# Performance work log

Measured on AMD Instinct MI355X. Metric: run time of the kernel, lower is better.

Reference implementation:

```python
import jax, jax.numpy as jnp
import numpy as np

B, R, H, W = 128, 8, 256, 256


def _conv(x, w, b):
    # x: [1, C_in, h, w], w: [C_out, C_in, 3, 3]; stride 2, pad 1, then bias + ReLU
    y = jax.lax.conv_general_dilated(
        x, w, window_strides=(2, 2), padding=((1, 1), (1, 1)),
        dimension_numbers=('NCHW', 'OIHW', 'NCHW'))
    return jax.nn.relu(y + b[None, :, None, None])


def _single(x, w1, b1, w2, b2, w3, b3, fw, fb):
    # x: [3, H, W]; one sample through its region's CNN expert
    h = x[None]                      # [1,3,H,W]
    h = _conv(h, w1, b1)             # [1,32,H/2,W/2]
    h = _conv(h, w2, b2)             # [1,64,H/4,W/4]
    h = _conv(h, w3, b3)             # [1,128,H/8,W/8]
    feat = h.mean(axis=(2, 3))[0]    # [128] global average pool
    return fw @ feat + fb            # [num_classes]


def setup_inputs() -> dict:
    key = jax.random.key(0)
    ks = jax.random.split(key, 10)
    s = 0.05
    return {
        'image': jax.random.normal(ks[0], (B, 3, H, W), jnp.float32),
        'region': jax.random.randint(ks[1], (B,), 0, R, jnp.int64),
        'w1': jax.random.normal(ks[2], (R, 32, 3, 3, 3), jnp.float32) * s,
        'b1': jax.random.normal(ks[3], (R, 32), jnp.float32) * s,
        'w2': jax.random.normal(ks[4], (R, 64, 32, 3, 3), jnp.float32) * s,
        'b2': jax.random.normal(ks[5], (R, 64), jnp.float32) * s,
        'w3': jax.random.normal(ks[6], (R, 128, 64, 3, 3), jnp.float32) * s,
        'b3': jax.random.normal(ks[7], (R, 128), jnp.float32) * s,
        'fw': jax.random.normal(ks[8], (R, 2, 128), jnp.float32) * s,
        'fb': jax.random.normal(ks[9], (R, 2), jnp.float32) * s,
    }


def reference(image, region, w1, b1, w2, b2, w3, b3, fw, fb):
    # MoE-style dispatch: gather each sample's region weights, vmap per-sample expert.
    r = region.astype(jnp.int32)
    pw = [jnp.take(p, r, axis=0) for p in (w1, b1, w2, b2, w3, b3, fw, fb)]
    out = jax.vmap(_single)(image, *pw)  # [B, num_classes]
    return out
```

## Files before the change

### kernel.cpp

```cpp
#include <hip/hip_runtime.h>
#include <cstdint>


typedef __attribute__((ext_vector_type(8))) short short8;
typedef __attribute__((ext_vector_type(4))) float floatx4;
typedef __attribute__((ext_vector_type(4))) unsigned short ushort4v;
typedef __attribute__((ext_vector_type(4))) float float4v;

__device__ inline unsigned short f2bf(float f) {
  union { float f; unsigned u; } x;
  x.f = f;
  unsigned u = x.u;
  u += 0x7FFFu + ((u >> 16) & 1u);
  return (unsigned short)(u >> 16);
}

__device__ inline void g2l16(const unsigned short* g, unsigned short* l) {
  __builtin_amdgcn_global_load_lds(
      (const __attribute__((address_space(1))) unsigned int*)g,
      (__attribute__((address_space(3))) unsigned int*)(unsigned int)(uintptr_t)l,
      16, 0, 0);
}

__global__ __launch_bounds__(256) void setup_k(
    const int* __restrict__ rp, int* __restrict__ rout, float* __restrict__ feat,
    const float* __restrict__ w1, unsigned short* __restrict__ w1p,
    const float* __restrict__ w2, unsigned short* __restrict__ w2p,
    const float* __restrict__ w3, unsigned short* __restrict__ w3p,
    unsigned short* __restrict__ h2p, int nhalo) {
  const int tid = threadIdx.x;
  if (blockIdx.x == 0) {
    __shared__ int is64;
    if (tid == 0) {
      int odd_or = 0;
      for (int i = 0; i < 64; ++i) odd_or |= rp[2 * i + 1];
      is64 = (odd_or == 0) ? 1 : 0;
    }
    __syncthreads();
    if (tid < 128) {
      int r = is64 ? rp[2 * tid] : rp[tid];
      rout[tid] = r & 7;
      float* fr = feat + tid * 128;
      for (int j = 0; j < 128; ++j) fr[j] = 0.f;
    }
    return;
  }
  int t = (blockIdx.x - 1) * 256 + tid;
  if (t < 16384) {
    int j = t & 7, lane = (t >> 3) & 63, mt = (t >> 9) & 1, kg = (t >> 10) & 1,
        r = t >> 11;
    int oc = mt * 16 + (lane & 15);
    int q = (lane >> 4) & 3;
    int row = kg * 2 + (q >> 1);
    int idx = (q & 1) * 8 + j;
    int kx = idx >> 2, c = idx & 3;
    float val = 0.f;
    if (row < 3 && kx < 3 && c < 3)
      val = w1[((r * 32 + oc) * 3 + c) * 9 + row * 3 + kx];
    w1p[t] = f2bf(val);
  } else if (t < 163840) {
    int t2 = t - 16384;
    int j = t2 & 7, lane = (t2 >> 3) & 63;
    int u = t2 >> 9;
    int mt = u & 3; u >>= 2;
    int tap = u % 9;
    int r = u / 9;
    int oc = mt * 16 + (lane & 15);
    int ic = ((lane >> 4) & 3) * 8 + j;
    w2p[t2] = f2bf(w2[((r * 64 + oc) * 32 + ic) * 9 + tap]);
  } else if (t < 753664) {
    int t3 = t - 163840;
    int j = t3 & 7, lane = (t3 >> 3) & 63;
    int u = t3 >> 9;
    int mt = u & 7; u >>= 3;
    int s = u & 1; u >>= 1;
    int tap = u % 9;
    int r = u / 9;
    int oc = mt * 16 + (lane & 15);
    int ic = s * 32 + ((lane >> 4) & 3) * 8 + j;
    w3p[t3] = f2bf(w3[((r * 128 + oc) * 64 + ic) * 9 + tap]);
  } else {
    int th = t - 753664;
    if (th < nhalo) {
      int s = th / 260, i = th - s * 260;
      int y, x;
      if (i < 66) { y = 0; x = i; }
      else if (i < 132) { y = 65; x = i - 66; }
      else {
        int ii = i - 132;
        y = 1 + (ii >> 1);
        x = (ii & 1) ? 65 : 0;
      }
      short8 z = {0, 0, 0, 0, 0, 0, 0, 0};
      *(short8*)(h2p + ((size_t)s * 66 * 66 + y * 66 + x) * 8) = z;
    }
  }
}

__global__ __launch_bounds__(256, 3) void conv12_k(
    const float* __restrict__ img, const unsigned short* __restrict__ w1p,
    const float* __restrict__ b1, const unsigned short* __restrict__ w2p,
    const float* __restrict__ b2, const int* __restrict__ rgn,
    unsigned short* __restrict__ outp, int b0) {
  __shared__ unsigned short imgT[11 * 168 * 4];
  __shared__ unsigned short h1T[9 * 4 * 66 * 8];
  __shared__ float sB1[32];
  __shared__ float sB2[64];
  const int tid = threadIdx.x;
  const int xh = blockIdx.x;
  const int oy0 = blockIdx.y * 4;
  const int bl = blockIdx.z;
  const int r = __builtin_amdgcn_readfirstlane(rgn[b0 + bl]);
  if (tid < 32) sB1[tid] = b1[r * 32 + tid];
  if (tid >= 64 && tid < 128) sB2[tid - 64] = b2[r * 64 + (tid - 64)];
  const float* ib = img + (size_t)(b0 + bl) * 3 * 65536;
  const int padx = xh ? 65 : 0;
  const bool skiptop = (oy0 == 0);
  const int rb = xh * 128 - 4;

  const int n = tid & 15, q = (tid >> 4) & 3, wv = tid >> 6;
  const int lane = tid & 63;
  const short8* wpb1 = (const short8*)w1p + (size_t)r * 256 + lane;
  short8 afr1[2][2];
#pragma unroll
  for (int kg = 0; kg < 2; ++kg)
#pragma unroll
    for (int m = 0; m < 2; ++m) afr1[kg][m] = wpb1[(kg * 2 + m) * 64];

  auto STAGE = [&](int t0, int nrows) {
    const int nch = nrows * 41;
    for (int seg = 0; seg < nch; seg += 256) {
      int c = seg + tid;
      if (c < nch) {
        int i = c / 41, cq = c - i * 41;
        int rv = 4 * oy0 - 3 + t0 + i;
        int cb = rb + 4 * cq;
        unsigned short* dp = &imgT[((size_t)i * 168 + (4 * cq - 1)) * 4];
        if (rv >= 0 && cq > 0 && cb >= 0 && cb + 3 <= 255) {
          const float* p = ib + (size_t)rv * 256 + cb;
          float4v a = *(const float4v*)p;
          float4v bb = *(const float4v*)(p + 65536);
          float4v cc = *(const float4v*)(p + 131072);
#pragma unroll
          for (int e = 0; e < 4; ++e) {
            ushort4v v = {f2bf(a[e]), f2bf(bb[e]), f2bf(cc[e]), 0};
            *(ushort4v*)(dp + e * 4) = v;
          }
        } else {
          for (int e = (cq == 0 ? 1 : 0); e < 4; ++e) {
            int cc2 = cb + e;
            ushort4v v = {0, 0, 0, 0};
            if (rv >= 0 && cc2 >= 0 && cc2 <= 255) {
              const float* p = ib + (size_t)rv * 256 + cc2;
              v.x = f2bf(p[0]);
              v.y = f2bf(p[65536]);
              v.z = f2bf(p[131072]);
            }
            *(ushort4v*)(dp + e * 4) = v;
          }
        }
      }
    }
  };

  auto CONV1ROW = [&](int hy, int phaseB) {
    floatx4 a1[5][2];
#pragma unroll
    for (int nt = 0; nt < 5; ++nt)
#pragma unroll
      for (int m = 0; m < 2; ++m) a1[nt][m] = (floatx4){0.f, 0.f, 0.f, 0.f};
#pragma unroll
    for (int kg = 0; kg < 2; ++kg) {
      int row = kg * 2 + (q >> 1);
      int rowc = (row < 3) ? row : 0;
      int tr = 2 * hy + rowc;
      int slot = phaseB ? (tr >= 11 ? tr - 11 : tr) : tr;
#pragma unroll
      for (int nt = 0; nt < 5; ++nt) {
        int lx = nt * 16 + n;
        short8 bfr = *(const short8*)&imgT[((size_t)slot * 168 + 2 * lx) * 4 +
                                           (q & 1) * 8];
#pragma unroll
        for (int m = 0; m < 2; ++m)
          a1[nt][m] = __builtin_amdgcn_mfma_f32_16x16x32_bf16(
              afr1[kg][m], bfr, a1[nt][m], 0, 0, 0);
      }
    }
#pragma unroll
    for (int nt = 0; nt < 5; ++nt) {
      int lx = nt * 16 + n;
      bool ok = (lx <= 65) && (lx != padx) && !(skiptop && hy == 0);
      if (ok) {
#pragma unroll
        for (int m = 0; m < 2; ++m) {
          ushort4v st;
#pragma unroll
          for (int rr = 0; rr < 4; ++rr) {
            float v = a1[nt][m][rr] + sB1[m * 16 + q * 4 + rr];
            st[rr] = f2bf(v > 0.f ? v : 0.f);
          }
          int cg = m * 2 + (q >> 1);
          *(ushort4v*)&h1T[(((size_t)hy * 4 + cg) * 66 + lx) * 8 +
                           (q & 1) * 4] = st;
        }
      }
    }
  };

  STAGE(0, 11);
  {
    short8 z8 = {0, 0, 0, 0, 0, 0, 0, 0};
    if (tid < 36) {
      int hy = tid / 4, cg = tid % 4;
      *(short8*)&h1T[(((size_t)hy * 4 + cg) * 66 + padx) * 8] = z8;
    }
    if (skiptop) {
      for (int c = tid; c < 264; c += 256) {
        int cg = c / 66, x = c - cg * 66;
        *(short8*)&h1T[(((size_t)0 * 4 + cg) * 66 + x) * 8] = z8;
      }
    }
  }
  __syncthreads();

  for (int hy = wv; hy <= 4; hy += 4) CONV1ROW(hy, 0);
  __syncthreads();

  STAGE(11, 8);
  __syncthreads();

  CONV1ROW(5 + wv, 1);
  __syncthreads();

  const short8* wpb2 = (const short8*)w2p + (size_t)r * 9 * 4 * 64 + lane;
  floatx4 a2[2][4];
#pragma unroll
  for (int nt = 0; nt < 2; ++nt)
#pragma unroll
    for (int m = 0; m < 4; ++m) a2[nt][m] = (floatx4){0.f, 0.f, 0.f, 0.f};
#pragma unroll
  for (int tap = 0; tap < 9; ++tap) {
    const int ky = tap / 3, kx = tap % 3;
    short8 af[4];
#pragma unroll
    for (int m = 0; m < 4; ++m) af[m] = wpb2[(tap * 4 + m) * 64];
    short8 bf[2];
#pragma unroll
    for (int nt = 0; nt < 2; ++nt) {
      int ox = nt * 16 + n;
      bf[nt] = *(const short8*)&h1T[((((2 * wv + ky) << 2) + q) * 66 +
                                    (2 * ox + kx)) * 8];
    }
#pragma unroll
    for (int m = 0; m < 4; ++m)
#pragma unroll
      for (int nt = 0; nt < 2; ++nt)
        a2[nt][m] = __builtin_amdgcn_mfma_f32_16x16x32_bf16(af[m], bf[nt],
                                                            a2[nt][m], 0, 0, 0);
  }
  unsigned short* ob = outp + (size_t)bl * 8 * 66 * 66 * 8;
  const int oy = oy0 + wv;
#pragma unroll
  for (int nt = 0; nt < 2; ++nt) {
    int ox = xh * 32 + nt * 16 + n;
#pragma unroll
    for (int m = 0; m < 4; ++m) {
      ushort4v st;
#pragma unroll
      for (int rr = 0; rr < 4; ++rr) {
        float v = a2[nt][m][rr] + sB2[m * 16 + q * 4 + rr];
        st[rr] = f2bf(v > 0.f ? v : 0.f);
      }
      int cg = m * 2 + (q >> 1);
      *(ushort4v*)&ob[(((size_t)cg * 66 + oy + 1) * 66 + ox + 1) * 8 +
                      (q & 1) * 4] = st;
    }
  }
}

__global__ __launch_bounds__(256, 2) void conv3f_k(
    const unsigned short* __restrict__ in, const unsigned short* __restrict__ wp,
    const float* __restrict__ bias, const int* __restrict__ rgn,
    float* __restrict__ feat, int b0) {
  __shared__ unsigned short tile[9 * 8 * 66 * 8];
  __shared__ float sBias[128];
  __shared__ float sGap[4 * 128];
  const int tid = threadIdx.x;
  const int bl = blockIdx.y;
  const int b = b0 + bl;
  const int r = __builtin_amdgcn_readfirstlane(rgn[b]);
  if (tid < 128) sBias[tid] = bias[r * 128 + tid];
  const int oy0 = blockIdx.x * 4;
  const unsigned short* gbase = in + (size_t)bl * 8 * 66 * 66 * 8;
  const int lane = tid & 63, wv = tid >> 6;
  const int n = lane & 15, q = (lane >> 4) & 3;

  for (int seg = 0; seg < 4752; seg += 256) {
    int c = seg + tid;
    if (c < 4752) {
      int iy = c / 528;
      int rem = c - iy * 528;
      int c8 = rem / 66;
      int x = rem - c8 * 66;
      const unsigned short* gp =
          gbase + (((size_t)c8 * 66 + 2 * oy0 + iy) * 66 + x) * 8;
      g2l16(gp, tile + (size_t)(seg + wv * 64) * 8);
    }
  }
  __syncthreads();

  const short8* wpb = (const short8*)wp + (size_t)r * 9 * 2 * 8 * 64 + lane;
  floatx4 acc[2][8];
#pragma unroll
  for (int nt = 0; nt < 2; ++nt)
#pragma unroll
    for (int m = 0; m < 8; ++m) acc[nt][m] = (floatx4){0.f, 0.f, 0.f, 0.f};

#pragma unroll
  for (int s = 0; s < 2; ++s)
#pragma unroll
    for (int tap = 0; tap < 9; ++tap) {
      const int ky = tap / 3, kx = tap % 3;
      short8 afr[8];
#pragma unroll
      for (int m = 0; m < 8; ++m) afr[m] = wpb[((tap * 2 + s) * 8 + m) * 64];
      short8 bfr[2];
#pragma unroll
      for (int nt = 0; nt < 2; ++nt) {
        int ox = nt * 16 + n;
        bfr[nt] = *(const short8*)&tile[((((2 * wv + ky) * 8) + s * 4 + q) * 66 +
                                        (2 * ox + kx)) * 8];
      }
#pragma unroll
      for (int m = 0; m < 8; ++m)
#pragma unroll
        for (int nt = 0; nt < 2; ++nt)
          acc[nt][m] = __builtin_amdgcn_mfma_f32_16x16x32_bf16(afr[m], bfr[nt],
                                                               acc[nt][m], 0, 0, 0);
    }

#pragma unroll
  for (int m = 0; m < 8; ++m)
#pragma unroll
    for (int rr = 0; rr < 4; ++rr) {
      float bv = sBias[m * 16 + q * 4 + rr];
      float vs = 0.f;
#pragma unroll
      for (int nt = 0; nt < 2; ++nt) {
        float v = acc[nt][m][rr] + bv;
        vs += (v > 0.f ? v : 0.f);
      }
      vs += __shfl_xor(vs, 1, 16);
      vs += __shfl_xor(vs, 2, 16);
      vs += __shfl_xor(vs, 4, 16);
      vs += __shfl_xor(vs, 8, 16);
      if (n == 0) sGap[wv * 128 + m * 16 + q * 4 + rr] = vs;
    }
  __syncthreads();
  if (tid < 128)
    atomicAdd(&feat[b * 128 + tid],
              sGap[tid] + sGap[128 + tid] + sGap[256 + tid] + sGap[384 + tid]);
}

__global__ __launch_bounds__(256) void head_k(
    const float* __restrict__ feat, const float* __restrict__ fw,
    const float* __restrict__ fb, const int* __restrict__ rgn,
    float* __restrict__ out) {
  int t = threadIdx.x;
  int b = t >> 1, c = t & 1;
  int r = rgn[b];
  const float* fwr = fw + (r * 2 + c) * 128;
  const float* fv = feat + b * 128;
  float a = 0.f;
#pragma unroll 8
  for (int j = 0; j < 128; ++j) a = fmaf(fwr[j], fv[j], a);
  out[t] = a * (1.0f / 1024.0f) + fb[r * 2 + c];
}

extern "C" void kernel_launch(void* const* d_in, const int* in_sizes, int n_in,
                              void* d_out, int out_size, void* d_ws, size_t ws_size,
                              hipStream_t stream) {
  const float* img = (const float*)d_in[0];
  const int* rgn_raw = (const int*)d_in[1];
  const float* w1 = (const float*)d_in[2];
  const float* b1 = (const float*)d_in[3];
  const float* w2 = (const float*)d_in[4];
  const float* b2 = (const float*)d_in[5];
  const float* w3 = (const float*)d_in[6];
  const float* b3 = (const float*)d_in[7];
  const float* fw = (const float*)d_in[8];
  const float* fb = (const float*)d_in[9];
  float* out = (float*)d_out;

  const size_t h2p_s = (size_t)8 * 66 * 66 * 8 * 2;
  const size_t per_sample = h2p_s;
  const size_t fixed = (size_t)16384 * 2 + (size_t)147456 * 2 +
                       (size_t)589824 * 2 + 128 * 128 * 4 + 512 + 16 * 256;
  int C = 128;
  while (C > 1 && fixed + (size_t)C * per_sample > ws_size) C >>= 1;

  char* ws = (char*)d_ws;
  size_t off = 0;
  auto alloc = [&](size_t bytes) {
    char* p = ws + off;
    off += (bytes + 255) & ~(size_t)255;
    return p;
  };
  unsigned short* h2p = (unsigned short*)alloc((size_t)C * h2p_s);
  unsigned short* w1p = (unsigned short*)alloc((size_t)16384 * 2);
  unsigned short* w2p = (unsigned short*)alloc((size_t)147456 * 2);
  unsigned short* w3p = (unsigned short*)alloc((size_t)589824 * 2);
  float* feat = (float*)alloc((size_t)128 * 128 * 4);
  int* rgn = (int*)alloc((size_t)128 * 4);

  {
    int nhalo = C * 8 * 260;
    int total = 753664 + nhalo;
    int nblk = 1 + (total + 255) / 256;
    hipLaunchKernelGGL(setup_k, dim3(nblk), dim3(256), 0, stream,
                       rgn_raw, rgn, feat, w1, w1p, w2, w2p, w3, w3p, h2p, nhalo);
  }

  for (int b0 = 0; b0 < 128; b0 += C) {
    hipLaunchKernelGGL(conv12_k, dim3(2, 16, C), dim3(256), 0, stream,
                       img, w1p, b1, w2p, b2, rgn, h2p, b0);
    hipLaunchKernelGGL(conv3f_k, dim3(8, C), dim3(256), 0, stream,
                       h2p, w3p, b3, rgn, feat, b0);
  }
  hipLaunchKernelGGL(head_k, dim3(1), dim3(256), 0, stream, feat, fw, fb, rgn, out);
}
```

Before: 300.5 us.

## Prefetch second image stage into registers and split conv3 tile loads

In conv12_k, the second batch of input rows is now loaded from global memory into registers before the first conv1 pass, then converted and stored to shared memory afterward, so global latency hides behind MFMA work. In the conv3 kernel, the shared tile is split into two channel halves. The second half is loaded asynchronously while the first half is computed. This adds register pressure and shared-memory layout changes in exchange for overlapping loads with compute.

Measured after the change: 293.1 us. 2.5% less time.

```diff
diff --git a/kernel.cpp b/kernel.cpp
--- a/kernel.cpp
+++ b/kernel.cpp
@@ -127,13 +127,13 @@
 #pragma unroll
     for (int m = 0; m < 2; ++m) afr1[kg][m] = wpb1[(kg * 2 + m) * 64];
 
-  auto STAGE = [&](int t0, int nrows) {
-    const int nch = nrows * 41;
+  {
+    const int nch = 11 * 41;
     for (int seg = 0; seg < nch; seg += 256) {
       int c = seg + tid;
       if (c < nch) {
         int i = c / 41, cq = c - i * 41;
-        int rv = 4 * oy0 - 3 + t0 + i;
+        int rv = 4 * oy0 - 3 + i;
         int cb = rb + 4 * cq;
         unsigned short* dp = &imgT[((size_t)i * 168 + (4 * cq - 1)) * 4];
         if (rv >= 0 && cq > 0 && cb >= 0 && cb + 3 <= 255) {
@@ -161,7 +161,20 @@
         }
       }
     }
-  };
+  }
+  {
+    short8 z8 = {0, 0, 0, 0, 0, 0, 0, 0};
+    if (tid < 36) {
+      int hy = tid / 4, cg = tid % 4;
+      *(short8*)&h1T[(((size_t)hy * 4 + cg) * 66 + padx) * 8] = z8;
+    }
+    if (skiptop) {
+      for (int c = tid; c < 264; c += 256) {
+        int cg = c / 66, x = c - cg * 66;
+        *(short8*)&h1T[(((size_t)0 * 4 + cg) * 66 + x) * 8] = z8;
+      }
+    }
+  }
 
   auto CONV1ROW = [&](int hy, int phaseB) {
     floatx4 a1[5][2];
@@ -207,26 +220,64 @@
     }
   };
 
-  STAGE(0, 11);
+  __syncthreads();
+
+  float4v Lb0[3], Lb1[3];
+  int ok0 = 0, ok1 = 0;
   {
-    short8 z8 = {0, 0, 0, 0, 0, 0, 0, 0};
-    if (tid < 36) {
-      int hy = tid / 4, cg = tid % 4;
-      *(short8*)&h1T[(((size_t)hy * 4 + cg) * 66 + padx) * 8] = z8;
-    }
-    if (skiptop) {
-      for (int c = tid; c < 264; c += 256) {
-        int cg = c / 66, x = c - cg * 66;
-        *(short8*)&h1T[(((size_t)0 * 4 + cg) * 66 + x) * 8] = z8;
-      }
-    }
-  }
-  __syncthreads();
+    int c = tid;
+    int i = c / 41, cq = c - i * 41;
+    int cb = rb + 4 * cq;
+    if (cq > 0 && cb >= 0 && cb + 3 <= 255) {
+      const float* p = ib + (size_t)(4 * oy0 + 8 + i) * 256 + cb;
+      Lb0[0] = *(const float4v*)p;
+      Lb0[1] = *(const float4v*)(p + 65536);
+      Lb0[2] = *(const float4v*)(p + 131072);
+      ok0 = 1;
+    }
+    c = tid + 256;
+    if (c < 328) {
+      i = c / 41; cq = c - i * 41; cb = rb + 4 * cq;
+      if (cq > 0 && cb >= 0 && cb + 3 <= 255) {
+        const float* p = ib + (size_t)(4 * oy0 + 8 + i) * 256 + cb;
+        Lb1[0] = *(const float4v*)p;
+        Lb1[1] = *(const float4v*)(p + 65536);
+        Lb1[2] = *(const float4v*)(p + 131072);
+        ok1 = 1;
+      }
+    }
+  }
 
   for (int hy = wv; hy <= 4; hy += 4) CONV1ROW(hy, 0);
   __syncthreads();
 
-  STAGE(11, 8);
+  auto STOREB = [&](int c, const float4v* L, int okf) {
+    int i = c / 41, cq = c - i * 41;
+    int cb = rb + 4 * cq;
+    unsigned short* dp = &imgT[((size_t)i * 168 + (4 * cq - 1)) * 4];
+    if (okf) {
+#pragma unroll
+      for (int e = 0; e < 4; ++e) {
+        ushort4v v = {f2bf(L[0][e]), f2bf(L[1][e]), f2bf(L[2][e]), 0};
+        *(ushort4v*)(dp + e * 4) = v;
+      }
+    } else {
+      int rv = 4 * oy0 + 8 + i;
+      for (int e = (cq == 0 ? 1 : 0); e < 4; ++e) {
+        int cc2 = cb + e;
+        ushort4v v = {0, 0, 0, 0};
+        if (cc2 >= 0 && cc2 <= 255) {
+          const float* p = ib + (size_t)rv * 256 + cc2;
+          v.x = f2bf(p[0]);
+          v.y = f2bf(p[65536]);
+          v.z = f2bf(p[131072]);
+        }
+        *(ushort4v*)(dp + e * 4) = v;
+      }
+    }
+  };
+  STOREB(tid, Lb0, ok0);
+  if (tid + 256 < 328) STOREB(tid + 256, Lb1, ok1);
   __syncthreads();
 
   CONV1ROW(5 + wv, 1);
@@ -278,11 +329,11 @@
   }
 }
 
-__global__ __launch_bounds__(256, 2) void conv3f_k(
+__global__ __launch_bounds__(256, 2) void conv3d_k(
     const unsigned short* __restrict__ in, const unsigned short* __restrict__ wp,
     const float* __restrict__ bias, const int* __restrict__ rgn,
     float* __restrict__ feat, int b0) {
-  __shared__ unsigned short tile[9 * 8 * 66 * 8];
+  __shared__ unsigned short tile[2][9 * 4 * 66 * 8];
   __shared__ float sBias[128];
   __shared__ float sGap[4 * 128];
   const int tid = threadIdx.x;
@@ -295,19 +346,20 @@
   const int lane = tid & 63, wv = tid >> 6;
   const int n = lane & 15, q = (lane >> 4) & 3;
 
-  for (int seg = 0; seg < 4752; seg += 256) {
-    int c = seg + tid;
-    if (c < 4752) {
-      int iy = c / 528;
-      int rem = c - iy * 528;
-      int c8 = rem / 66;
-      int x = rem - c8 * 66;
-      const unsigned short* gp =
-          gbase + (((size_t)c8 * 66 + 2 * oy0 + iy) * 66 + x) * 8;
-      g2l16(gp, tile + (size_t)(seg + wv * 64) * 8);
-    }
-  }
-  __syncthreads();
+  auto STG = [&](int s) {
+    for (int seg = 0; seg < 2376; seg += 256) {
+      int c = seg + tid;
+      if (c < 2376) {
+        int iy = c / 264;
+        int rem = c - iy * 264;
+        int c8 = rem / 66;
+        int x = rem - c8 * 66;
+        const unsigned short* gp =
+            gbase + (((size_t)(s * 4 + c8) * 66 + 2 * oy0 + iy) * 66 + x) * 8;
+        g2l16(gp, tile[s] + (size_t)(seg + wv * 64) * 8);
+      }
+    }
+  };
 
   const short8* wpb = (const short8*)wp + (size_t)r * 9 * 2 * 8 * 64 + lane;
   floatx4 acc[2][8];
@@ -316,8 +368,7 @@
 #pragma unroll
     for (int m = 0; m < 8; ++m) acc[nt][m] = (floatx4){0.f, 0.f, 0.f, 0.f};
 
-#pragma unroll
-  for (int s = 0; s < 2; ++s)
+  auto COMPUTE = [&](int s) {
 #pragma unroll
     for (int tap = 0; tap < 9; ++tap) {
       const int ky = tap / 3, kx = tap % 3;
@@ -328,8 +379,8 @@
 #pragma unroll
       for (int nt = 0; nt < 2; ++nt) {
         int ox = nt * 16 + n;
-        bfr[nt] = *(const short8*)&tile[((((2 * wv + ky) * 8) + s * 4 + q) * 66 +
-                                        (2 * ox + kx)) * 8];
+        bfr[nt] = *(const short8*)&tile[s][(((2 * wv + ky) * 4 + q) * 66 +
+                                          (2 * ox + kx)) * 8];
       }
 #pragma unroll
       for (int m = 0; m < 8; ++m)
@@ -338,6 +389,14 @@
           acc[nt][m] = __builtin_amdgcn_mfma_f32_16x16x32_bf16(afr[m], bfr[nt],
                                                                acc[nt][m], 0, 0, 0);
     }
+  };
+
+  STG(0);
+  __syncthreads();
+  STG(1);
+  COMPUTE(0);
+  __syncthreads();
+  COMPUTE(1);
 
 #pragma unroll
   for (int m = 0; m < 8; ++m)
@@ -424,7 +483,7 @@
   for (int b0 = 0; b0 < 128; b0 += C) {
     hipLaunchKernelGGL(conv12_k, dim3(2, 16, C), dim3(256), 0, stream,
                        img, w1p, b1, w2p, b2, rgn, h2p, b0);
-    hipLaunchKernelGGL(conv3f_k, dim3(8, C), dim3(256), 0, stream,
+    hipLaunchKernelGGL(conv3d_k, dim3(8, C), dim3(256), 0, stream,
                        h2p, w3p, b3, rgn, feat, b0);
   }
   hipLaunchKernelGGL(head_k, dim3(1), dim3(256), 0, stream, feat, fw, fb, rgn, out);
```
